# Kernel tuning notes

Hardware: AMD Instinct MI355X
Metric: run time of the kernel (lower is better)

## Reference

```python
import jax, jax.numpy as jnp
import numpy as np

D_MODEL, N_HEADS, D_C, D_COMP, D_ROPE = 2048, 16, 512, 768, 64
D_HEAD = D_MODEL // N_HEADS  # 128
B, S = 2, 2048
ROPE_THETA = 10000.0


def _rope_cos_sin(seq_len, dim):
    # frequencies for pairwise complex rotation, dim = per-head rope dim (even)
    inv_freq = 1.0 / (ROPE_THETA ** (jnp.arange(0, dim, 2, dtype=jnp.float32) / dim))
    t = jnp.arange(seq_len, dtype=jnp.float32)
    ang = t[:, None] * inv_freq[None, :]  # [S, dim/2]
    return jnp.cos(ang), jnp.sin(ang)


def _apply_rope(x, cos, sin):
    # x: [B, S, H, dr]; rotate consecutive pairs (view_as_complex semantics)
    x1, x2 = x[..., 0::2], x[..., 1::2]
    c = cos[None, :, None, :]
    s = sin[None, :, None, :]
    y1 = x1 * c - x2 * s
    y2 = x1 * s + x2 * c
    return jnp.stack([y1, y2], axis=-1).reshape(x.shape)


def setup_inputs() -> dict:
    key = jax.random.key(0)
    ks = jax.random.split(key, 9)
    sc = 0.02
    return {
        "x": jax.random.normal(ks[0], (B, S, D_MODEL), jnp.float32),
        "Wd": jax.random.normal(ks[1], (D_MODEL, D_C), jnp.float32) * sc,
        "bd": jnp.zeros((D_C,), jnp.float32),
        "Wu": jax.random.normal(ks[2], (D_C, N_HEADS * D_HEAD), jnp.float32) * sc,
        "bu": jnp.zeros((N_HEADS * D_HEAD,), jnp.float32),
        "Wqd": jax.random.normal(ks[3], (D_MODEL, D_COMP), jnp.float32) * sc,
        "bqd": jnp.zeros((D_COMP,), jnp.float32),
        "Wqu": jax.random.normal(ks[4], (D_COMP, N_HEADS * D_HEAD), jnp.float32) * sc,
        "bqu": jnp.zeros((N_HEADS * D_HEAD,), jnp.float32),
        "Wqr": jax.random.normal(ks[5], (D_COMP, N_HEADS * D_ROPE), jnp.float32) * sc,
        "bqr": jnp.zeros((N_HEADS * D_ROPE,), jnp.float32),
        "Wkr": jax.random.normal(ks[6], (D_MODEL, N_HEADS * D_ROPE), jnp.float32) * sc,
        "bkr": jnp.zeros((N_HEADS * D_ROPE,), jnp.float32),
        "Wo": jax.random.normal(ks[7], (N_HEADS * D_HEAD, D_MODEL), jnp.float32) * sc,
        "bo": jnp.zeros((D_MODEL,), jnp.float32),
    }


def reference(x, Wd, bd, Wu, bu, Wqd, bqd, Wqu, bqu, Wqr, bqr, Wkr, bkr, Wo, bo):
    b, s, _ = x.shape
    # low-rank KV compression
    kv_c = x @ Wd + bd                                   # [B,S,d_c]
    kv_up = (kv_c @ Wu + bu).reshape(b, s, N_HEADS, D_HEAD)  # shared K-content / V
    # low-rank Q compression
    q_cmp = x @ Wqd + bqd                                # [B,S,d_comp]
    q_c = (q_cmp @ Wqu + bqu).reshape(b, s, N_HEADS, D_HEAD)
    # decoupled RoPE branches
    cos, sin = _rope_cos_sin(s, D_ROPE)
    q_r = _apply_rope((q_cmp @ Wqr + bqr).reshape(b, s, N_HEADS, D_ROPE), cos, sin)
    k_r = _apply_rope((x @ Wkr + bkr).reshape(b, s, N_HEADS, D_ROPE), cos, sin)
    q = jnp.concatenate([q_c, q_r], axis=-1)             # [B,S,H,dh+dr]
    k = jnp.concatenate([kv_up, k_r], axis=-1)           # [B,S,H,dh+dr]
    scale = 1.0 / np.sqrt(D_HEAD).astype(np.float32)
    scores = jnp.einsum('bqhd,bkhd->bhqk', q, k) * scale  # [B,H,S,S]
    probs = jax.nn.softmax(scores, axis=-1)
    out = jnp.einsum('bhqk,bkhd->bqhd', probs, kv_up)    # v == kv_up (as in source)
    out = out.reshape(b, s, N_HEADS * D_HEAD)
    return out @ Wo + bo
```

## Files before the change

kernel.cpp:

```cpp
#include <hip/hip_runtime.h>
#include <cmath>

typedef __bf16 bf16;
typedef __bf16 bf16x8 __attribute__((ext_vector_type(8)));
typedef __bf16 bf16x4 __attribute__((ext_vector_type(4)));
typedef __bf16 bf16x2 __attribute__((ext_vector_type(2)));
typedef float f32x4 __attribute__((ext_vector_type(4)));
typedef float f32x16 __attribute__((ext_vector_type(16)));
typedef int i32x4 __attribute__((ext_vector_type(4)));
typedef int i32x2 __attribute__((ext_vector_type(2)));

#define S_LEN 2048
#define QK_LD 3072

__device__ __forceinline__ void async_copy16(const bf16* g, bf16* l) {
    __builtin_amdgcn_global_load_lds(
        (const __attribute__((address_space(1))) void*)g,
        (__attribute__((address_space(3))) void*)l, 16, 0, 0);
}

__device__ __forceinline__ unsigned packbf(float a, float b) {
    bf16x2 v; v[0] = (bf16)a; v[1] = (bf16)b;
    return __builtin_bit_cast(unsigned, v);
}

__global__ __launch_bounds__(256) void cast_f32_bf16(const float* __restrict__ in,
                                                     bf16* __restrict__ out) {
    size_t i = ((size_t)blockIdx.x * 256 + threadIdx.x) * 8;
    float4 a = *(const float4*)(in + i);
    float4 b = *(const float4*)(in + i + 4);
    bf16x8 v;
    v[0] = (bf16)a.x; v[1] = (bf16)a.y; v[2] = (bf16)a.z; v[3] = (bf16)a.w;
    v[4] = (bf16)b.x; v[5] = (bf16)b.y; v[6] = (bf16)b.z; v[7] = (bf16)b.w;
    *(bf16x8*)(out + i) = v;
}

struct TSeg { const float* src; bf16* dst; int K, N, blk0; };
struct TArgs { TSeg s[7]; };

__global__ __launch_bounds__(256) void transpose_all(TArgs a) {
    __shared__ float tile[64][68];
    int b = blockIdx.x, si = 0;
#pragma unroll
    for (int i = 1; i < 7; ++i) if (b >= a.s[i].blk0) si = i;
    TSeg sg = a.s[si];
    int local = b - sg.blk0;
    int kTiles = sg.K >> 6;
    int kt = local % kTiles, nt = local / kTiles;
    int k0 = kt * 64, n0 = nt * 64;
    int K = sg.K, N = sg.N;
    int t = threadIdx.x;
#pragma unroll
    for (int i = 0; i < 4; ++i) {
        int c = t + i * 256;
        int r = c >> 4, off = (c & 15) * 4;
        float4 v = *(const float4*)(sg.src + (size_t)(k0 + r) * N + n0 + off);
        tile[r][off] = v.x; tile[r][off + 1] = v.y;
        tile[r][off + 2] = v.z; tile[r][off + 3] = v.w;
    }
    __syncthreads();
#pragma unroll
    for (int i = 0; i < 2; ++i) {
        int c = t + i * 256;
        int nr = c >> 3, koff = (c & 7) * 8;
        bf16x8 v;
#pragma unroll
        for (int j = 0; j < 8; ++j) v[j] = (bf16)tile[koff + j][nr];
        *(bf16x8*)(sg.dst + (size_t)(n0 + nr) * K + k0 + koff) = v;
    }
}

__global__ __launch_bounds__(256) void setup_small(const float* __restrict__ bd,
                                                   const float* __restrict__ bqd,
                                                   const float* __restrict__ bkr,
                                                   const float* __restrict__ bqu,
                                                   const float* __restrict__ bqr,
                                                   float* __restrict__ bcat,
                                                   float2* __restrict__ tab) {
    if (blockIdx.x < 21) {
        int i = blockIdx.x * 256 + threadIdx.x;
        if (i < 512) bcat[i] = bd[i];
        else if (i < 1280) bcat[i] = bqd[i - 512];
        else if (i < 2304) bcat[i] = bkr[i - 1280];
        else if (i < 4352) bcat[i] = bqu[i - 2304];
        else if (i < 5376) bcat[i] = bqr[i - 4352];
    } else {
        int id = (blockIdx.x - 21) * 256 + threadIdx.x;
        int s = id >> 5, i = id & 31;
        float f = expf(-0.2878231366242557f * (float)i);
        float ang = (float)s * f;
        tab[id] = make_float2(cosf(ang), sinf(ang));
    }
}

__device__ __forceinline__ void gemm_core(const bf16* __restrict__ A, int lda,
                                          const bf16* __restrict__ Bt,
                                          const float* __restrict__ bias,
                                          void* __restrict__ out0,
                                          void* __restrict__ out1,
                                          int Ndim, int Kdim, int mode,
                                          const float2* __restrict__ tab,
                                          int bn, int bm, bf16* As, bf16* Bs) {
    int t = threadIdx.x;
    int w = t >> 6, lane = t & 63;
    int wm = (w >> 1) * 64, wn = (w & 1) * 64;
    int l15 = lane & 15, q4 = lane >> 4;
    f32x4 acc[4][4] = {};

    int lrow = lane >> 2;
    int lcol = (lane & 3) * 8;
    int c0 = w * 2, c1 = w * 2 + 1;
    const bf16* aS0 = A  + (size_t)(bm * 128 + c0 * 16 + lrow) * lda + lcol;
    const bf16* aS1 = A  + (size_t)(bm * 128 + c1 * 16 + lrow) * lda + lcol;
    const bf16* bS0 = Bt + (size_t)(bn * 128 + c0 * 16 + lrow) * Kdim + lcol;
    const bf16* bS1 = Bt + (size_t)(bn * 128 + c1 * 16 + lrow) * Kdim + lcol;
    bf16* aD0 = &As[c0 * 512]; bf16* aD1 = &As[c1 * 512];
    bf16* bD0 = &Bs[c0 * 512]; bf16* bD1 = &Bs[c1 * 512];

    for (int kt = 0; kt < Kdim; kt += 32) {
        async_copy16(aS0 + kt, aD0);
        async_copy16(aS1 + kt, aD1);
        async_copy16(bS0 + kt, bD0);
        async_copy16(bS1 + kt, bD1);
        __syncthreads();
        bf16x8 af[4], bfr[4];
#pragma unroll
        for (int mb = 0; mb < 4; ++mb)
            af[mb] = *(const bf16x8*)&As[(wm + mb * 16 + l15) * 32 + q4 * 8];
#pragma unroll
        for (int nb = 0; nb < 4; ++nb)
            bfr[nb] = *(const bf16x8*)&Bs[(wn + nb * 16 + l15) * 32 + q4 * 8];
#pragma unroll
        for (int mb = 0; mb < 4; ++mb)
#pragma unroll
            for (int nb = 0; nb < 4; ++nb)
                acc[mb][nb] = __builtin_amdgcn_mfma_f32_16x16x32_bf16(
                    af[mb], bfr[nb], acc[mb][nb], 0, 0, 0);
        __syncthreads();
    }

#pragma unroll
    for (int mb = 0; mb < 4; ++mb) {
        int row = bm * 128 + wm + mb * 16 + q4 * 4;
#pragma unroll
        for (int nb = 0; nb < 4; ++nb) {
            int col = bn * 128 + wn + nb * 16 + l15;
            float bv = bias[col];
            if (mode == 1) {
#pragma unroll
                for (int r = 0; r < 4; ++r)
                    ((float*)out0)[(size_t)(row + r) * Ndim + col] = acc[mb][nb][r] + bv;
            } else if (mode == 4) {
                if (col < 1280) {
#pragma unroll
                    for (int r = 0; r < 4; ++r)
                        ((bf16*)out0)[(size_t)(row + r) * 2304 + col] =
                            (bf16)(acc[mb][nb][r] + bv);
                } else {
                    int rel = col - 1280;
                    int hh = rel >> 6, idx = rel & 63, ii = idx >> 1, odd = idx & 1;
#pragma unroll
                    for (int r = 0; r < 4; ++r) {
                        float vv = acc[mb][nb][r] + bv;
                        float pp = __shfl_xor(vv, 1, 64);
                        float2 cs = tab[((row + r) & 2047) * 32 + ii];
                        float o = vv * cs.x + (odd ? pp * cs.y : -pp * cs.y);
                        ((bf16*)out1)[(size_t)(row + r) * QK_LD + hh * 192 + 128 + idx] =
                            (bf16)o;
                    }
                }
            } else if (mode == 5) {
                if (col < 2048) {
                    int hh = col >> 7, dd = col & 127;
#pragma unroll
                    for (int r = 0; r < 4; ++r)
                        ((bf16*)out0)[(size_t)(row + r) * QK_LD + hh * 192 + dd] =
                            (bf16)(acc[mb][nb][r] + bv);
                } else {
                    int rel = col - 2048;
                    int hh = rel >> 6, idx = rel & 63, ii = idx >> 1, odd = idx & 1;
#pragma unroll
                    for (int r = 0; r < 4; ++r) {
                        float vv = acc[mb][nb][r] + bv;
                        float pp = __shfl_xor(vv, 1, 64);
                        float2 cs = tab[((row + r) & 2047) * 32 + ii];
                        float o = vv * cs.x + (odd ? pp * cs.y : -pp * cs.y);
                        ((bf16*)out0)[(size_t)(row + r) * QK_LD + hh * 192 + 128 + idx] =
                            (bf16)o;
                    }
                }
            } else {
                int hh = col >> 7, dd = col & 127;
                bf16x4 pack;
#pragma unroll
                for (int r = 0; r < 4; ++r) {
                    float vv = acc[mb][nb][r] + bv;
                    ((bf16*)out0)[(size_t)(row + r) * QK_LD + hh * 192 + dd] = (bf16)vv;
                    pack[r] = (bf16)vv;
                }
                int bidx = row >> 11, srow = row & 2047;
                *(bf16x4*)((bf16*)out1 +
                           ((size_t)(bidx * 16 + hh) * 128 + dd) * S_LEN + srow) = pack;
            }
        }
    }
}

__global__ __launch_bounds__(256) void gemm_bt(const bf16* __restrict__ A, int lda,
                                               const bf16* __restrict__ Bt,
                                               const float* __restrict__ bias,
                                               void* __restrict__ out0,
                                               void* __restrict__ out1,
                                               int Ndim, int Kdim, int mode,
                                               const float2* __restrict__ tab) {
    __shared__ bf16 As[128 * 32];
    __shared__ bf16 Bs[128 * 32];
    gemm_core(A, lda, Bt, bias, out0, out1, Ndim, Kdim, mode, tab,
              blockIdx.x, blockIdx.y, As, Bs);
}

__global__ __launch_bounds__(256) void gemm_up(const bf16* __restrict__ xproj,
                                               const bf16* __restrict__ WuT,
                                               const float* __restrict__ bu,
                                               void* __restrict__ kbuf,
                                               void* __restrict__ vt,
                                               const bf16* __restrict__ W2T,
                                               const float* __restrict__ bq,
                                               void* __restrict__ qbuf,
                                               const float2* __restrict__ tab) {
    __shared__ bf16 As[128 * 32];
    __shared__ bf16 Bs[128 * 32];
    int bn = blockIdx.x;
    if (bn < 16)
        gemm_core(xproj, 2304, WuT, bu, kbuf, vt, 2048, 512, 6, tab,
                  bn, blockIdx.y, As, Bs);
    else
        gemm_core(xproj + 512, 2304, W2T, bq, qbuf, nullptr, 3072, 768, 5, tab,
                  bn - 16, blockIdx.y, As, Bs);
}

__global__ __launch_bounds__(256, 1) void attn(const bf16* __restrict__ qbuf,
                                               const bf16* __restrict__ kbuf,
                                               const bf16* __restrict__ vt,
                                               bf16* __restrict__ attnout) {
    __shared__ bf16 Ks[2][32 * 192];
    __shared__ bf16 Vs[2][128 * 32];
    int bh = blockIdx.x;
    int qt = blockIdx.y;
    int b = bh >> 4, h = bh & 15;
    int t = threadIdx.x, w = t >> 6, lane = t & 63;
    int l31 = lane & 31, hl = lane >> 5;
    const float scale = 0.08838834764831845f;

    bf16x8 qf[2][12];
#pragma unroll
    for (int qg = 0; qg < 2; ++qg) {
        size_t rbase = (size_t)(b * S_LEN + qt * 256 + w * 64 + qg * 32 + l31) * QK_LD
                       + h * 192 + hl * 8;
#pragma unroll
        for (int c = 0; c < 12; ++c)
            qf[qg][c] = *(const bf16x8*)(qbuf + rbase + c * 16);
    }

    f32x16 oacc[2][4] = {};
    float denom[2] = {0.f, 0.f};
    const bf16* kb_base = kbuf + (size_t)b * S_LEN * QK_LD + h * 192;
    const bf16* vt_base = vt + (size_t)bh * 128 * S_LEN;

    int kg_[3], klA_[3], klB_[3];
#pragma unroll
    for (int i = 0; i < 3; ++i) {
        int c = t + (i << 8);
        int kr = c / 24, u = c % 24;
        kg_[i] = kr * QK_LD + u * 8;
        int m = kr & 15;
        klA_[i] = kr * 192 + (((2 * u) ^ m) << 2);
        klB_[i] = kr * 192 + (((2 * u + 1) ^ m) << 2);
    }
    int vg_[2], vlA_[2], vlB_[2];
#pragma unroll
    for (int i = 0; i < 2; ++i) {
        int c = t + (i << 8);
        int vd = c >> 2, u = c & 3;
        vg_[i] = vd * S_LEN + u * 8;
        int line = vd >> 1, lm = line & 15;
        int sl = 8 * (vd & 1) + 2 * u;
        vlA_[i] = line * 64 + ((sl ^ lm) << 2);
        vlB_[i] = line * 64 + (((sl + 1) ^ lm) << 2);
    }

    int mK = l31 & 15;
    int kRow = l31 * 192;
    int vLM = l31 >> 1;
    int vSlotB = 8 * (l31 & 1) + 2 * hl;

    i32x4 kreg[3], vreg[2];
#pragma unroll
    for (int i = 0; i < 3; ++i) kreg[i] = *(const i32x4*)(kb_base + kg_[i]);
#pragma unroll
    for (int i = 0; i < 2; ++i) vreg[i] = *(const i32x4*)(vt_base + vg_[i]);
#pragma unroll
    for (int i = 0; i < 3; ++i) {
        i32x2 lo; lo[0] = kreg[i][0]; lo[1] = kreg[i][1];
        i32x2 hi; hi[0] = kreg[i][2]; hi[1] = kreg[i][3];
        *(i32x2*)&Ks[0][klA_[i]] = lo;
        *(i32x2*)&Ks[0][klB_[i]] = hi;
    }
#pragma unroll
    for (int i = 0; i < 2; ++i) {
        i32x2 lo; lo[0] = vreg[i][0]; lo[1] = vreg[i][1];
        i32x2 hi; hi[0] = vreg[i][2]; hi[1] = vreg[i][3];
        *(i32x2*)&Vs[0][vlA_[i]] = lo;
        *(i32x2*)&Vs[0][vlB_[i]] = hi;
    }
    __syncthreads();

    int cur = 0;
    for (int kt = 0; kt < 64; ++kt) {
        if (kt < 63) {
            const bf16* kb = kb_base + (size_t)(kt + 1) * 32 * QK_LD;
#pragma unroll
            for (int i = 0; i < 3; ++i) kreg[i] = *(const i32x4*)(kb + kg_[i]);
#pragma unroll
            for (int i = 0; i < 2; ++i)
                vreg[i] = *(const i32x4*)(vt_base + (kt + 1) * 32 + vg_[i]);
        }

        f32x16 sacc[2] = {};
#pragma unroll
        for (int c = 0; c < 12; ++c) {
            int u0 = 4 * c + 2 * hl;
            i32x2 lo = *(const i32x2*)&Ks[cur][kRow + ((u0 ^ mK) << 2)];
            i32x2 hi = *(const i32x2*)&Ks[cur][kRow + (((u0 + 1) ^ mK) << 2)];
            i32x4 kv; kv[0] = lo[0]; kv[1] = lo[1]; kv[2] = hi[0]; kv[3] = hi[1];
            bf16x8 kb = __builtin_bit_cast(bf16x8, kv);
            sacc[0] = __builtin_amdgcn_mfma_f32_32x32x16_bf16(kb, qf[0][c], sacc[0], 0, 0, 0);
            sacc[1] = __builtin_amdgcn_mfma_f32_32x32x16_bf16(kb, qf[1][c], sacc[1], 0, 0, 0);
        }

        bf16x8 paf[2][2];
#pragma unroll
        for (int qg = 0; qg < 2; ++qg) {
            unsigned W[8], pw[8];
#pragma unroll
            for (int m = 0; m < 8; ++m) {
                float e0 = __expf(fminf(sacc[qg][2 * m] * scale, 50.0f));
                float e1 = __expf(fminf(sacc[qg][2 * m + 1] * scale, 50.0f));
                denom[qg] += e0 + e1;
                W[m] = packbf(e0, e1);
            }
#pragma unroll
            for (int m = 0; m < 8; ++m)
                pw[m] = (unsigned)__shfl_xor((int)W[m], 32, 64);
#pragma unroll
            for (int s = 0; s < 2; ++s) {
                unsigned A = hl ? pw[4 * s + 2] : W[4 * s + 0];
                unsigned B = hl ? pw[4 * s + 3] : W[4 * s + 1];
                unsigned C = hl ? W[4 * s + 2] : pw[4 * s + 0];
                unsigned D = hl ? W[4 * s + 3] : pw[4 * s + 1];
                i32x4 di; di[0] = (int)A; di[1] = (int)B; di[2] = (int)C; di[3] = (int)D;
                paf[qg][s] = __builtin_bit_cast(bf16x8, di);
            }
        }

#pragma unroll
        for (int dg = 0; dg < 4; ++dg) {
#pragma unroll
            for (int s = 0; s < 2; ++s) {
                int line = dg * 16 + (l31 >> 1);
                int s0 = (vSlotB + 4 * s) ^ vLM;
                int s1 = (vSlotB + 4 * s + 1) ^ vLM;
                i32x2 lo = *(const i32x2*)&Vs[cur][line * 64 + (s0 << 2)];
                i32x2 hi = *(const i32x2*)&Vs[cur][line * 64 + (s1 << 2)];
                i32x4 vv; vv[0] = lo[0]; vv[1] = lo[1]; vv[2] = hi[0]; vv[3] = hi[1];
                bf16x8 vb = __builtin_bit_cast(bf16x8, vv);
                oacc[0][dg] = __builtin_amdgcn_mfma_f32_32x32x16_bf16(
                    paf[0][s], vb, oacc[0][dg], 0, 0, 0);
                oacc[1][dg] = __builtin_amdgcn_mfma_f32_32x32x16_bf16(
                    paf[1][s], vb, oacc[1][dg], 0, 0, 0);
            }
        }

        if (kt < 63) {
#pragma unroll
            for (int i = 0; i < 3; ++i) {
                i32x2 lo; lo[0] = kreg[i][0]; lo[1] = kreg[i][1];
                i32x2 hi; hi[0] = kreg[i][2]; hi[1] = kreg[i][3];
                *(i32x2*)&Ks[cur ^ 1][klA_[i]] = lo;
                *(i32x2*)&Ks[cur ^ 1][klB_[i]] = hi;
            }
#pragma unroll
            for (int i = 0; i < 2; ++i) {
                i32x2 lo; lo[0] = vreg[i][0]; lo[1] = vreg[i][1];
                i32x2 hi; hi[0] = vreg[i][2]; hi[1] = vreg[i][3];
                *(i32x2*)&Vs[cur ^ 1][vlA_[i]] = lo;
                *(i32x2*)&Vs[cur ^ 1][vlB_[i]] = hi;
            }
        }
        __syncthreads();
        cur ^= 1;
    }

    denom[0] += __shfl_xor(denom[0], 32, 64);
    denom[1] += __shfl_xor(denom[1], 32, 64);

#pragma unroll
    for (int qg = 0; qg < 2; ++qg)
#pragma unroll
        for (int r = 0; r < 16; ++r) {
            int rowl = (r & 3) + 8 * (r >> 2) + 4 * hl;
            float dv = __shfl(denom[qg], rowl, 64);
            float inv = 1.0f / dv;
            int row = qt * 256 + w * 64 + qg * 32 + rowl;
#pragma unroll
            for (int dg = 0; dg < 4; ++dg) {
                int col = h * 128 + dg * 32 + l31;
                attnout[(size_t)(b * S_LEN + row) * 2048 + col] =
                    (bf16)(oacc[qg][dg][r] * inv);
            }
        }
}

extern "C" void kernel_launch(void* const* d_in, const int* in_sizes, int n_in,
                              void* d_out, int out_size, void* d_ws, size_t ws_size,
                              hipStream_t stream) {
    const float* x   = (const float*)d_in[0];
    const float* Wd  = (const float*)d_in[1];
    const float* bd  = (const float*)d_in[2];
    const float* Wu  = (const float*)d_in[3];
    const float* bu  = (const float*)d_in[4];
    const float* Wqd = (const float*)d_in[5];
    const float* bqd = (const float*)d_in[6];
    const float* Wqu = (const float*)d_in[7];
    const float* bqu = (const float*)d_in[8];
    const float* Wqr = (const float*)d_in[9];
    const float* bqr = (const float*)d_in[10];
    const float* Wkr = (const float*)d_in[11];
    const float* bkr = (const float*)d_in[12];
    const float* Wo  = (const float*)d_in[13];
    const float* bo  = (const float*)d_in[14];
    float* out = (float*)d_out;

    char* p = (char*)d_ws;
    auto alloc = [&](size_t n) { char* r = p; p += (n + 255) & ~(size_t)255; return r; };
    bf16* xb    = (bf16*)alloc((size_t)4096 * 2048 * 2);
    bf16* W1T   = (bf16*)alloc((size_t)2304 * 2048 * 2);
    bf16* W2T   = (bf16*)alloc((size_t)3072 * 768 * 2);
    bf16* WuT   = (bf16*)alloc((size_t)2048 * 512 * 2);
    bf16* WoT   = (bf16*)alloc((size_t)2048 * 2048 * 2);
    bf16* xproj = (bf16*)alloc((size_t)4096 * 2304 * 2);
    bf16* qbuf  = (bf16*)alloc((size_t)4096 * 3072 * 2);
    bf16* kbuf  = (bf16*)alloc((size_t)4096 * 3072 * 2);
    bf16* vt    = (bf16*)alloc((size_t)32 * 128 * 2048 * 2);
    bf16* aout  = (bf16*)alloc((size_t)4096 * 2048 * 2);
    float* bcat = (float*)alloc((size_t)5376 * 4);
    float2* tab = (float2*)alloc((size_t)65536 * 8);

    cast_f32_bf16<<<dim3(4096), dim3(256), 0, stream>>>(x, xb);

    TArgs ta;
    ta.s[0] = {Wd,  W1T,                       2048, 512,  0};
    ta.s[1] = {Wqd, W1T + (size_t)512 * 2048,  2048, 768,  256};
    ta.s[2] = {Wkr, W1T + (size_t)1280 * 2048, 2048, 1024, 640};
    ta.s[3] = {Wqu, W2T,                       768,  2048, 1152};
    ta.s[4] = {Wqr, W2T + (size_t)2048 * 768,  768,  1024, 1536};
    ta.s[5] = {Wu,  WuT,                       512,  2048, 1728};
    ta.s[6] = {Wo,  WoT,                       2048, 2048, 1984};
    transpose_all<<<dim3(3008), dim3(256), 0, stream>>>(ta);
    setup_small<<<dim3(277), dim3(256), 0, stream>>>(bd, bqd, bkr, bqu, bqr, bcat, tab);

    gemm_bt<<<dim3(18, 32), dim3(256), 0, stream>>>(xb, 2048, W1T, bcat,
                                                    xproj, kbuf, 2304, 2048, 4, tab);
    gemm_up<<<dim3(40, 32), dim3(256), 0, stream>>>(xproj, WuT, bu, kbuf, vt,
                                                    W2T, bcat + 2304, qbuf, tab);

    attn<<<dim3(32, 8), dim3(256), 0, stream>>>(qbuf, kbuf, vt, aout);

    gemm_bt<<<dim3(16, 32), dim3(256), 0, stream>>>(aout, 2048, WoT, bo,
                                                    out, nullptr, 2048, 2048, 1, tab);
}
```

Baseline: 465.0 us.

## Halve attention query tile, raise occupancy, add XCD-aware GEMM block remap

Each attention block now covers 128 queries instead of 256, with one 32-row query group per wave, and the grid doubles to 512 blocks with launch bounds allowing two blocks per CU. The aim is better occupancy and load balance on a 256-CU part, at the cost of loading each K/V tile twice as often. MFMA sections are wrapped in s_setprio, and exp is computed as exp2 with a pre-folded log2e scale. The GEMM kernels also remap block indices so consecutive tiles land on the same XCD, which is meant to improve L2 reuse.

Result: faster. 434.8 us (-6.5%).

```diff
diff --git a/kernel.cpp b/kernel.cpp
--- a/kernel.cpp
+++ b/kernel.cpp
@@ -206,6 +206,15 @@
     }
 }
 
+__device__ __forceinline__ void xcd_chunk(int gx, int& bn, int& bm) {
+    int lin = blockIdx.y * gx + blockIdx.x;
+    int nwg = gx * gridDim.y;
+    int chunk = nwg >> 3;
+    int nl = (lin & 7) * chunk + (lin >> 3);
+    bn = nl % gx;
+    bm = nl / gx;
+}
+
 __global__ __launch_bounds__(256) void gemm_bt(const bf16* __restrict__ A, int lda,
                                                const bf16* __restrict__ Bt,
                                                const float* __restrict__ bias,
@@ -215,8 +224,10 @@
                                                const float2* __restrict__ tab) {
     __shared__ bf16 As[128 * 32];
     __shared__ bf16 Bs[128 * 32];
+    int bn, bm;
+    xcd_chunk(gridDim.x, bn, bm);
     gemm_core(A, lda, Bt, bias, out0, out1, Ndim, Kdim, mode, tab,
-              blockIdx.x, blockIdx.y, As, Bs);
+              bn, bm, As, Bs);
 }
 
 __global__ __launch_bounds__(256) void gemm_up(const bf16* __restrict__ xproj,
@@ -230,16 +241,17 @@
                                                const float2* __restrict__ tab) {
     __shared__ bf16 As[128 * 32];
     __shared__ bf16 Bs[128 * 32];
-    int bn = blockIdx.x;
+    int bn, bm;
+    xcd_chunk(gridDim.x, bn, bm);
     if (bn < 16)
         gemm_core(xproj, 2304, WuT, bu, kbuf, vt, 2048, 512, 6, tab,
-                  bn, blockIdx.y, As, Bs);
+                  bn, bm, As, Bs);
     else
         gemm_core(xproj + 512, 2304, W2T, bq, qbuf, nullptr, 3072, 768, 5, tab,
-                  bn - 16, blockIdx.y, As, Bs);
-}
-
-__global__ __launch_bounds__(256, 1) void attn(const bf16* __restrict__ qbuf,
+                  bn - 16, bm, As, Bs);
+}
+
+__global__ __launch_bounds__(256, 2) void attn(const bf16* __restrict__ qbuf,
                                                const bf16* __restrict__ kbuf,
                                                const bf16* __restrict__ vt,
                                                bf16* __restrict__ attnout) {
@@ -250,24 +262,23 @@
     int b = bh >> 4, h = bh & 15;
     int t = threadIdx.x, w = t >> 6, lane = t & 63;
     int l31 = lane & 31, hl = lane >> 5;
-    const float scale = 0.08838834764831845f;
-
-    bf16x8 qf[2][12];
-#pragma unroll
-    for (int qg = 0; qg < 2; ++qg) {
-        size_t rbase = (size_t)(b * S_LEN + qt * 256 + w * 64 + qg * 32 + l31) * QK_LD
+    const float scale2 = 0.1275174333f;
+
+    bf16x8 qf[12];
+    {
+        size_t rbase = (size_t)(b * S_LEN + qt * 128 + w * 32 + l31) * QK_LD
                        + h * 192 + hl * 8;
 #pragma unroll
         for (int c = 0; c < 12; ++c)
-            qf[qg][c] = *(const bf16x8*)(qbuf + rbase + c * 16);
-    }
-
-    f32x16 oacc[2][4] = {};
-    float denom[2] = {0.f, 0.f};
+            qf[c] = *(const bf16x8*)(qbuf + rbase + c * 16);
+    }
+
+    f32x16 oacc[4] = {};
+    float denom = 0.f;
     const bf16* kb_base = kbuf + (size_t)b * S_LEN * QK_LD + h * 192;
     const bf16* vt_base = vt + (size_t)bh * 128 * S_LEN;
 
-    int kg_[3], klA_[3], klB_[3];
+    int kg_[3], klA_[3], klB_[3], vg_[2], vlA_[2], vlB_[2];
 #pragma unroll
     for (int i = 0; i < 3; ++i) {
         int c = t + (i << 8);
@@ -277,7 +288,6 @@
         klA_[i] = kr * 192 + (((2 * u) ^ m) << 2);
         klB_[i] = kr * 192 + (((2 * u + 1) ^ m) << 2);
     }
-    int vg_[2], vlA_[2], vlB_[2];
 #pragma unroll
     for (int i = 0; i < 2; ++i) {
         int c = t + (i << 8);
@@ -326,7 +336,8 @@
                 vreg[i] = *(const i32x4*)(vt_base + (kt + 1) * 32 + vg_[i]);
         }
 
-        f32x16 sacc[2] = {};
+        f32x16 sacc = {};
+        __builtin_amdgcn_s_setprio(1);
 #pragma unroll
         for (int c = 0; c < 12; ++c) {
             int u0 = 4 * c + 2 * hl;
@@ -334,35 +345,33 @@
             i32x2 hi = *(const i32x2*)&Ks[cur][kRow + (((u0 + 1) ^ mK) << 2)];
             i32x4 kv; kv[0] = lo[0]; kv[1] = lo[1]; kv[2] = hi[0]; kv[3] = hi[1];
             bf16x8 kb = __builtin_bit_cast(bf16x8, kv);
-            sacc[0] = __builtin_amdgcn_mfma_f32_32x32x16_bf16(kb, qf[0][c], sacc[0], 0, 0, 0);
-            sacc[1] = __builtin_amdgcn_mfma_f32_32x32x16_bf16(kb, qf[1][c], sacc[1], 0, 0, 0);
-        }
-
-        bf16x8 paf[2][2];
-#pragma unroll
-        for (int qg = 0; qg < 2; ++qg) {
-            unsigned W[8], pw[8];
-#pragma unroll
-            for (int m = 0; m < 8; ++m) {
-                float e0 = __expf(fminf(sacc[qg][2 * m] * scale, 50.0f));
-                float e1 = __expf(fminf(sacc[qg][2 * m + 1] * scale, 50.0f));
-                denom[qg] += e0 + e1;
-                W[m] = packbf(e0, e1);
-            }
-#pragma unroll
-            for (int m = 0; m < 8; ++m)
-                pw[m] = (unsigned)__shfl_xor((int)W[m], 32, 64);
-#pragma unroll
-            for (int s = 0; s < 2; ++s) {
-                unsigned A = hl ? pw[4 * s + 2] : W[4 * s + 0];
-                unsigned B = hl ? pw[4 * s + 3] : W[4 * s + 1];
-                unsigned C = hl ? W[4 * s + 2] : pw[4 * s + 0];
-                unsigned D = hl ? W[4 * s + 3] : pw[4 * s + 1];
-                i32x4 di; di[0] = (int)A; di[1] = (int)B; di[2] = (int)C; di[3] = (int)D;
-                paf[qg][s] = __builtin_bit_cast(bf16x8, di);
-            }
-        }
-
+            sacc = __builtin_amdgcn_mfma_f32_32x32x16_bf16(kb, qf[c], sacc, 0, 0, 0);
+        }
+        __builtin_amdgcn_s_setprio(0);
+
+        unsigned W[8], pw[8];
+#pragma unroll
+        for (int m = 0; m < 8; ++m) {
+            float e0 = __builtin_amdgcn_exp2f(fminf(sacc[2 * m] * scale2, 72.0f));
+            float e1 = __builtin_amdgcn_exp2f(fminf(sacc[2 * m + 1] * scale2, 72.0f));
+            denom += e0 + e1;
+            W[m] = packbf(e0, e1);
+        }
+#pragma unroll
+        for (int m = 0; m < 8; ++m)
+            pw[m] = (unsigned)__shfl_xor((int)W[m], 32, 64);
+        bf16x8 paf[2];
+#pragma unroll
+        for (int s = 0; s < 2; ++s) {
+            unsigned A = hl ? pw[4 * s + 2] : W[4 * s + 0];
+            unsigned B = hl ? pw[4 * s + 3] : W[4 * s + 1];
+            unsigned C = hl ? W[4 * s + 2] : pw[4 * s + 0];
+            unsigned D = hl ? W[4 * s + 3] : pw[4 * s + 1];
+            i32x4 di; di[0] = (int)A; di[1] = (int)B; di[2] = (int)C; di[3] = (int)D;
+            paf[s] = __builtin_bit_cast(bf16x8, di);
+        }
+
+        __builtin_amdgcn_s_setprio(1);
 #pragma unroll
         for (int dg = 0; dg < 4; ++dg) {
 #pragma unroll
@@ -374,12 +383,11 @@
                 i32x2 hi = *(const i32x2*)&Vs[cur][line * 64 + (s1 << 2)];
                 i32x4 vv; vv[0] = lo[0]; vv[1] = lo[1]; vv[2] = hi[0]; vv[3] = hi[1];
                 bf16x8 vb = __builtin_bit_cast(bf16x8, vv);
-                oacc[0][dg] = __builtin_amdgcn_mfma_f32_32x32x16_bf16(
-                    paf[0][s], vb, oacc[0][dg], 0, 0, 0);
-                oacc[1][dg] = __builtin_amdgcn_mfma_f32_32x32x16_bf16(
-                    paf[1][s], vb, oacc[1][dg], 0, 0, 0);
+                oacc[dg] = __builtin_amdgcn_mfma_f32_32x32x16_bf16(
+                    paf[s], vb, oacc[dg], 0, 0, 0);
             }
         }
+        __builtin_amdgcn_s_setprio(0);
 
         if (kt < 63) {
 #pragma unroll
@@ -401,24 +409,21 @@
         cur ^= 1;
     }
 
-    denom[0] += __shfl_xor(denom[0], 32, 64);
-    denom[1] += __shfl_xor(denom[1], 32, 64);
-
-#pragma unroll
-    for (int qg = 0; qg < 2; ++qg)
-#pragma unroll
-        for (int r = 0; r < 16; ++r) {
-            int rowl = (r & 3) + 8 * (r >> 2) + 4 * hl;
-            float dv = __shfl(denom[qg], rowl, 64);
-            float inv = 1.0f / dv;
-            int row = qt * 256 + w * 64 + qg * 32 + rowl;
-#pragma unroll
-            for (int dg = 0; dg < 4; ++dg) {
-                int col = h * 128 + dg * 32 + l31;
-                attnout[(size_t)(b * S_LEN + row) * 2048 + col] =
-                    (bf16)(oacc[qg][dg][r] * inv);
-            }
-        }
+    denom += __shfl_xor(denom, 32, 64);
+
+#pragma unroll
+    for (int r = 0; r < 16; ++r) {
+        int rowl = (r & 3) + 8 * (r >> 2) + 4 * hl;
+        float dv = __shfl(denom, rowl, 64);
+        float inv = 1.0f / dv;
+        int row = qt * 128 + w * 32 + rowl;
+#pragma unroll
+        for (int dg = 0; dg < 4; ++dg) {
+            int col = h * 128 + dg * 32 + l31;
+            attnout[(size_t)(b * S_LEN + row) * 2048 + col] =
+                (bf16)(oacc[dg][r] * inv);
+        }
+    }
 }
 
 extern "C" void kernel_launch(void* const* d_in, const int* in_sizes, int n_in,
@@ -474,7 +479,7 @@
     gemm_up<<<dim3(40, 32), dim3(256), 0, stream>>>(xproj, WuT, bu, kbuf, vt,
                                                     W2T, bcat + 2304, qbuf, tab);
 
-    attn<<<dim3(32, 8), dim3(256), 0, stream>>>(qbuf, kbuf, vt, aout);
+    attn<<<dim3(32, 16), dim3(256), 0, stream>>>(qbuf, kbuf, vt, aout);
 
     gemm_bt<<<dim3(16, 32), dim3(256), 0, stream>>>(aout, 2048, WoT, bo,
                                                     out, nullptr, 2048, 2048, 1, tab);
```
